# Performance work log

Measured on AMD Instinct MI355X. Metric: run time of the kernel, lower is better.

Reference implementation:

```python
import jax, jax.numpy as jnp
import numpy as np

# Model dims
B, S, D = 2, 1024, 1024          # batch, seq, d_model
NH, HD = 16, 64                  # n_heads, head_dim
E, K, H = 8, 2, 4096             # num_experts, experts_per_token, expert hidden
EPS = 1e-6
ROPE_BASE = 10000.0


def rmsnorm(x, w):
    # RMSNorm: x * rsqrt(mean(x^2) + eps) * weight (no mean-centering, no bias)
    return x * jax.lax.rsqrt(jnp.mean(x * x, axis=-1, keepdims=True) + EPS) * w


def apply_rope(q, k):
    # q,k: [B, NH, S, HD]; position_ids = arange(S) broadcast over batch
    hd = q.shape[-1]
    s = q.shape[2]
    inv_freq = 1.0 / (ROPE_BASE ** (jnp.arange(0, hd, 2, dtype=jnp.float32) / hd))
    freqs = jnp.arange(s, dtype=jnp.float32)[:, None] * inv_freq          # [S, HD/2]
    emb = jnp.concatenate([freqs, freqs], axis=-1)                        # [S, HD]
    cos = jnp.cos(emb)[None, None]                                        # [1,1,S,HD]
    sin = jnp.sin(emb)[None, None]

    def rotate_half(x):
        x1, x2 = jnp.split(x, 2, axis=-1)
        return jnp.concatenate([-x2, x1], axis=-1)

    return q * cos + rotate_half(q) * sin, k * cos + rotate_half(k) * sin


def setup_inputs() -> dict:
    key = jax.random.key(0)
    ks = jax.random.split(key, 9)
    sc = 0.02
    return {
        "x": jax.random.normal(ks[0], (B, S, D), jnp.float32),
        "attn_norm_w": jnp.ones((D,), jnp.float32),
        "wq": jax.random.normal(ks[1], (D, D), jnp.float32) * sc,
        "wk": jax.random.normal(ks[2], (D, D), jnp.float32) * sc,
        "wv": jax.random.normal(ks[3], (D, D), jnp.float32) * sc,
        "wo": jax.random.normal(ks[4], (D, D), jnp.float32) * sc,
        "moe_norm_w": jnp.ones((D,), jnp.float32),
        "gate_w": jax.random.normal(ks[5], (E, D), jnp.float32) * sc,
        "w1": jax.random.normal(ks[6], (E, H, D), jnp.float32) * sc,
        "b1": jnp.zeros((E, H), jnp.float32),
        "w2": jax.random.normal(ks[7], (E, D, H), jnp.float32) * sc,
        "b2": jnp.zeros((E, D), jnp.float32),
    }


def reference(x, attn_norm_w, wq, wk, wv, wo, moe_norm_w, gate_w, w1, b1, w2, b2):
    b, s, d = x.shape
    # --- pre-norm causal self-attention with RoPE (eval mode: no dropout) ---
    t = rmsnorm(x, attn_norm_w)
    q = (t @ wq.T).reshape(b, s, NH, HD).transpose(0, 2, 1, 3)
    k = (t @ wk.T).reshape(b, s, NH, HD).transpose(0, 2, 1, 3)
    v = (t @ wv.T).reshape(b, s, NH, HD).transpose(0, 2, 1, 3)
    q, k = apply_rope(q, k)
    scores = jnp.einsum("bhqd,bhkd->bhqk", q, k) / np.float32(np.sqrt(HD))
    causal = jnp.tril(jnp.ones((s, s), bool))
    scores = jnp.where(causal, scores, jnp.float32(-1e30))
    attn = jax.nn.softmax(scores, axis=-1)
    ao = jnp.einsum("bhqk,bhkd->bhqd", attn, v).transpose(0, 2, 1, 3).reshape(b, s, d)
    h = x + ao @ wo.T

    # --- sparse top-k MoE FFN (internal RMSNorm + residual) ---
    tn = rmsnorm(h, moe_norm_w).reshape(-1, d)                  # [T, D]
    logits = tn @ gate_w.T                                      # [T, E]
    gate_scores, idx = jax.lax.top_k(logits, K)                 # [T, K]
    rw = jax.nn.softmax(gate_scores, axis=-1)                   # [T, K]
    # compute all experts densely, then gather selected (same math as
    # gathering per-token expert weight matrices, far less memory traffic)
    hid = jax.nn.gelu(jnp.einsum("td,ehd->teh", tn, w1) + b1, approximate=False)
    eo = jnp.einsum("teh,edh->ted", hid, w2) + b2               # [T, E, D]
    sel = jnp.take_along_axis(eo, idx[:, :, None], axis=1)      # [T, K, D]
    moe_out = jnp.einsum("tkd,tk->td", sel, rw).reshape(b, s, d)
    return h + moe_out
```

## Files before the change

kernel.cpp:

```cpp
#include <hip/hip_runtime.h>
#include <hip/hip_bf16.h>
#include <hip/hip_fp16.h>


#define T_TOK 2048
#define DMODEL 1024
#define SEQ 1024
#define NEXP 8
#define HEXP 4096

typedef __attribute__((ext_vector_type(4))) float f32x4;
typedef __attribute__((ext_vector_type(4))) int i32x4;
typedef __attribute__((ext_vector_type(8))) short short8;
typedef __attribute__((ext_vector_type(8))) _Float16 half8;
typedef __attribute__((ext_vector_type(4))) _Float16 half4;

#define WAIT_VM3 asm volatile("s_waitcnt vmcnt(3)" ::: "memory")
#define WAIT_VM4 asm volatile("s_waitcnt vmcnt(4)" ::: "memory")
#define WAIT_VM6 asm volatile("s_waitcnt vmcnt(6)" ::: "memory")
#define WAIT_VM0 asm volatile("s_waitcnt vmcnt(0)" ::: "memory")
#define WAIT_LGKM0 asm volatile("s_waitcnt lgkmcnt(0)" ::: "memory")
#define BARRIER __builtin_amdgcn_s_barrier()
#define SCHEDFENCE __builtin_amdgcn_sched_barrier(0)

__device__ __forceinline__ void gload16(const void* g, void* l)
{
    __builtin_amdgcn_global_load_lds((const __attribute__((address_space(1))) void*)g,
                                     (__attribute__((address_space(3))) void*)l, 16, 0, 0);
}

__device__ __forceinline__ void bsplit(float f, unsigned short& hi, unsigned short& lo)
{
    unsigned int u = __float_as_uint(f);
    unsigned int rh = (u + 0x7FFFu + ((u >> 16) & 1u)) >> 16;
    hi = (unsigned short)rh;
    float fl = f - __uint_as_float(rh << 16);
    unsigned int u2 = __float_as_uint(fl);
    lo = (unsigned short)((u2 + 0x7FFFu + ((u2 >> 16) & 1u)) >> 16);
}

__device__ __forceinline__ float gelu_fast(float v)
{
    float e = __expf(-1.5957691216f * v * (1.0f + 0.044715f * v * v));
    return v * __builtin_amdgcn_rcpf(1.0f + e);
}

__global__ __launch_bounds__(256) void split4_kernel(
    const float* __restrict__ s0, const float* __restrict__ s1,
    const float* __restrict__ s2, const float* __restrict__ s3,
    unsigned short* __restrict__ h0, unsigned short* __restrict__ h1,
    unsigned short* __restrict__ h2, unsigned short* __restrict__ h3,
    unsigned short* __restrict__ l0, unsigned short* __restrict__ l1,
    unsigned short* __restrict__ l2, unsigned short* __restrict__ l3, int n4)
{
    int z = blockIdx.y;
    const float* src = (z == 0) ? s0 : (z == 1) ? s1 : (z == 2) ? s2 : s3;
    unsigned short* hi = (z == 0) ? h0 : (z == 1) ? h1 : (z == 2) ? h2 : h3;
    unsigned short* lo = (z == 0) ? l0 : (z == 1) ? l1 : (z == 2) ? l2 : l3;
    int stride = gridDim.x * blockDim.x;
    for (int i = blockIdx.x * blockDim.x + threadIdx.x; i < n4; i += stride) {
        float4 v = ((const float4*)src)[i];
        ushort4 h, l;
        bsplit(v.x, h.x, l.x); bsplit(v.y, h.y, l.y);
        bsplit(v.z, h.z, l.z); bsplit(v.w, h.w, l.w);
        *(ushort4*)(hi + (size_t)i * 4) = h;
        *(ushort4*)(lo + (size_t)i * 4) = l;
    }
}

__global__ __launch_bounds__(256) void rmsnorm_kernel(const float* __restrict__ x,
                                                      const float* __restrict__ w,
                                                      float* __restrict__ of,
                                                      _Float16* __restrict__ oh,
                                                      unsigned short* __restrict__ ohi,
                                                      unsigned short* __restrict__ olo)
{
    int row = blockIdx.x;
    int t = threadIdx.x;
    float4 v = ((const float4*)(x + (size_t)row * DMODEL))[t];
    float ss = v.x * v.x + v.y * v.y + v.z * v.z + v.w * v.w;
#pragma unroll
    for (int off = 32; off > 0; off >>= 1) ss += __shfl_xor(ss, off);
    __shared__ float red[4];
    if ((t & 63) == 0) red[t >> 6] = ss;
    __syncthreads();
    float tot = red[0] + red[1] + red[2] + red[3];
    float sc = rsqrtf(tot * (1.0f / DMODEL) + 1e-6f);
    float4 w4 = ((const float4*)w)[t];
    float4 o;
    o.x = v.x * sc * w4.x; o.y = v.y * sc * w4.y; o.z = v.z * sc * w4.z; o.w = v.w * sc * w4.w;
    if (of) ((float4*)(of + (size_t)row * DMODEL))[t] = o;
    if (oh) {
        half4 h = { (_Float16)o.x, (_Float16)o.y, (_Float16)o.z, (_Float16)o.w };
        *(half4*)(oh + (size_t)row * DMODEL + t * 4) = h;
    }
    if (ohi) {
        ushort4 h, l;
        bsplit(o.x, h.x, l.x); bsplit(o.y, h.y, l.y);
        bsplit(o.z, h.z, l.z); bsplit(o.w, h.w, l.w);
        *(ushort4*)(ohi + (size_t)row * DMODEL + t * 4) = h;
        *(ushort4*)(olo + (size_t)row * DMODEL + t * 4) = l;
    }
}

__global__ __launch_bounds__(256) void gemm_split_kernel(
    const unsigned short* __restrict__ aH, const unsigned short* __restrict__ aL,
    const unsigned short* __restrict__ b0H, const unsigned short* __restrict__ b0L,
    const unsigned short* __restrict__ b1H, const unsigned short* __restrict__ b1L,
    const unsigned short* __restrict__ b2H, const unsigned short* __restrict__ b2L,
    float* __restrict__ C0, float* __restrict__ C1, float* __restrict__ C2,
    const float* __restrict__ resid, int K)
{
    const unsigned short* bH = (blockIdx.z == 0) ? b0H : (blockIdx.z == 1 ? b1H : b2H);
    const unsigned short* bL = (blockIdx.z == 0) ? b0L : (blockIdx.z == 1 ? b1L : b2L);
    float* C = (blockIdx.z == 0) ? C0 : (blockIdx.z == 1 ? C1 : C2);
    int m0 = blockIdx.y * 128, n0 = blockIdx.x * 64;
    __shared__ unsigned short AsH[2][128 * 32];
    __shared__ unsigned short AsL[2][128 * 32];
    __shared__ unsigned short BsH[2][64 * 32];
    __shared__ unsigned short BsL[2][64 * 32];
    int t = threadIdx.x, w = t >> 6, l = t & 63;
    int sa = l >> 2, sc = (l & 3) * 8;
    const unsigned short* gAH0 = aH + (size_t)(m0 + w * 32 + sa) * K + sc;
    const unsigned short* gAH1 = aH + (size_t)(m0 + w * 32 + 16 + sa) * K + sc;
    const unsigned short* gAL0 = aL + (size_t)(m0 + w * 32 + sa) * K + sc;
    const unsigned short* gAL1 = aL + (size_t)(m0 + w * 32 + 16 + sa) * K + sc;
    const unsigned short* gBH0 = bH + (size_t)(n0 + w * 16 + sa) * K + sc;
    const unsigned short* gBL0 = bL + (size_t)(n0 + w * 16 + sa) * K + sc;
    const int aoff0 = (w * 32) * 32;
    const int aoff1 = (w * 32 + 16) * 32;
    const int boff0 = (w * 16) * 32;
    int wr = w >> 1, wc = w & 1;
    f32x4 zero = { 0.0f, 0.0f, 0.0f, 0.0f };
    f32x4 acc[4][2];
#pragma unroll
    for (int i = 0; i < 4; i++)
#pragma unroll
        for (int j = 0; j < 2; j++) acc[i][j] = zero;

#define GS_STAGE(B, K0) do { \
    gload16(gAH0 + (K0), &AsH[B][aoff0]); gload16(gAH1 + (K0), &AsH[B][aoff1]); \
    gload16(gAL0 + (K0), &AsL[B][aoff0]); gload16(gAL1 + (K0), &AsL[B][aoff1]); \
    gload16(gBH0 + (K0), &BsH[B][boff0]); gload16(gBL0 + (K0), &BsL[B][boff0]); \
} while (0)

#define GS_COMPUTE(B) do { \
    short8 ah[4], al[4], bh8[2], bl8[2]; \
    _Pragma("unroll") \
    for (int mi = 0; mi < 4; mi++) { \
        int base = (wr * 64 + mi * 16 + (l & 15)) * 32 + (l >> 4) * 8; \
        ah[mi] = *(const short8*)&AsH[B][base]; \
        al[mi] = *(const short8*)&AsL[B][base]; } \
    _Pragma("unroll") \
    for (int ni = 0; ni < 2; ni++) { \
        int base = (wc * 32 + ni * 16 + (l & 15)) * 32 + (l >> 4) * 8; \
        bh8[ni] = *(const short8*)&BsH[B][base]; \
        bl8[ni] = *(const short8*)&BsL[B][base]; } \
    _Pragma("unroll") \
    for (int mi = 0; mi < 4; mi++) \
        _Pragma("unroll") \
        for (int ni = 0; ni < 2; ni++) { \
            acc[mi][ni] = __builtin_amdgcn_mfma_f32_16x16x32_bf16(ah[mi], bh8[ni], acc[mi][ni], 0, 0, 0); \
            acc[mi][ni] = __builtin_amdgcn_mfma_f32_16x16x32_bf16(ah[mi], bl8[ni], acc[mi][ni], 0, 0, 0); \
            acc[mi][ni] = __builtin_amdgcn_mfma_f32_16x16x32_bf16(al[mi], bh8[ni], acc[mi][ni], 0, 0, 0); } \
} while (0)

    const int nt = K >> 5;
    GS_STAGE(0, 0);
    for (int kt = 0; kt < nt; kt += 2) {
        GS_STAGE(1, (kt + 1) << 5);
        WAIT_VM6;
        BARRIER; SCHEDFENCE;
        GS_COMPUTE(0);
        BARRIER;
        if (kt + 2 < nt) {
            GS_STAGE(0, (kt + 2) << 5);
            WAIT_VM6;
        } else {
            WAIT_VM0;
        }
        BARRIER; SCHEDFENCE;
        GS_COMPUTE(1);
        BARRIER;
    }
#undef GS_STAGE
#undef GS_COMPUTE

#pragma unroll
    for (int mi = 0; mi < 4; mi++) {
#pragma unroll
        for (int r = 0; r < 4; r++) {
            int row = m0 + wr * 64 + mi * 16 + (l >> 4) * 4 + r;
#pragma unroll
            for (int ni = 0; ni < 2; ni++) {
                int col = n0 + wc * 32 + ni * 16 + (l & 15);
                float v = acc[mi][ni][r];
                if (resid) v += resid[(size_t)row * DMODEL + col];
                C[(size_t)row * DMODEL + col] = v;
            }
        }
    }
}

__global__ __launch_bounds__(256) void rope_split_kernel(
    const float* __restrict__ qf, const float* __restrict__ kf,
    unsigned short* __restrict__ qHi, unsigned short* __restrict__ qLo,
    unsigned short* __restrict__ kHi, unsigned short* __restrict__ kLo)
{
    int i = blockIdx.x * 256 + threadIdx.x;
    int tok = i >> 9;
    int r = i & 511;
    int hh = r >> 5, ii = r & 31;
    int s = tok & (SEQ - 1);
    int b = tok >> 10;
    float invf = powf(10000.0f, -(float)(2 * ii) * (1.0f / 64.0f));
    float ang = (float)s * invf;
    float c = cosf(ang), sn = sinf(ang);
    size_t base = (size_t)tok * DMODEL + hh * 64 + ii;
    float q1 = qf[base], q2 = qf[base + 32];
    float k1 = kf[base], k2 = kf[base + 32];
    float rq1 = (q1 * c - q2 * sn) * 0.125f;
    float rq2 = (q2 * c + q1 * sn) * 0.125f;
    float rk1 = k1 * c - k2 * sn;
    float rk2 = k2 * c + k1 * sn;
    int bh = b * 16 + hh;
    size_t qb = ((size_t)bh * SEQ + s) * 64 + ii;
    unsigned short h, lo;
    bsplit(rq1, h, lo); qHi[qb] = h; qLo[qb] = lo;
    bsplit(rq2, h, lo); qHi[qb + 32] = h; qLo[qb + 32] = lo;
    size_t kb = (size_t)bh * (SEQ * 64) + (size_t)(s >> 6) * 4096 + (size_t)(s & 63) * 64;
    int d1 = ii, d2 = ii + 32;
    int p1 = (((d1 >> 3) ^ (s & 7)) << 3) | (d1 & 7);
    int p2 = (((d2 >> 3) ^ (s & 7)) << 3) | (d2 & 7);
    bsplit(rk1, h, lo); kHi[kb + p1] = h; kLo[kb + p1] = lo;
    bsplit(rk2, h, lo); kHi[kb + p2] = h; kLo[kb + p2] = lo;
}

__global__ __launch_bounds__(256) void vtrans_kernel(const float* __restrict__ vf,
                                                     unsigned short* __restrict__ vtHi,
                                                     unsigned short* __restrict__ vtLo)
{
    int sb = blockIdx.x, bh = blockIdx.y;
    int b = bh >> 4, h = bh & 15;
    __shared__ unsigned short tH[64][72];
    __shared__ unsigned short tL[64][72];
    int t = threadIdx.x;
#pragma unroll
    for (int i = 0; i < 4; i++) {
        int idx = i * 256 + t, row = idx >> 4, c4 = idx & 15;
        float4 v = *(const float4*)(vf + (size_t)(b * SEQ + sb * 64 + row) * DMODEL + h * 64 + c4 * 4);
        unsigned short hh, ll;
        bsplit(v.x, hh, ll); tH[c4 * 4 + 0][row] = hh; tL[c4 * 4 + 0][row] = ll;
        bsplit(v.y, hh, ll); tH[c4 * 4 + 1][row] = hh; tL[c4 * 4 + 1][row] = ll;
        bsplit(v.z, hh, ll); tH[c4 * 4 + 2][row] = hh; tL[c4 * 4 + 2][row] = ll;
        bsplit(v.w, hh, ll); tH[c4 * 4 + 3][row] = hh; tL[c4 * 4 + 3][row] = ll;
    }
    __syncthreads();
#pragma unroll
    for (int i = 0; i < 4; i++) {
        int idx = i * 256 + t, d = idx >> 4, sc4 = idx & 15;
        ushort4 oh = { tH[d][sc4 * 4 + 0], tH[d][sc4 * 4 + 1], tH[d][sc4 * 4 + 2], tH[d][sc4 * 4 + 3] };
        ushort4 ol = { tL[d][sc4 * 4 + 0], tL[d][sc4 * 4 + 1], tL[d][sc4 * 4 + 2], tL[d][sc4 * 4 + 3] };
        size_t off = (size_t)bh * (64 * SEQ) + (size_t)sb * 4096 + (size_t)d * 64
                   + (((sc4 >> 1) ^ (d & 7)) << 3) + ((sc4 & 1) << 2);
        *(ushort4*)(vtHi + off) = oh;
        *(ushort4*)(vtLo + off) = ol;
    }
}

__global__ __launch_bounds__(512) void attn_mfma_kernel(
    const unsigned short* __restrict__ qHi, const unsigned short* __restrict__ qLo,
    const unsigned short* __restrict__ kHi, const unsigned short* __restrict__ kLo,
    const unsigned short* __restrict__ vtHi, const unsigned short* __restrict__ vtLo,
    float* __restrict__ Opart, float* __restrict__ mscr, float* __restrict__ lscr)
{
    int qt = 7 - blockIdx.x;
    int bh = blockIdx.y, ks = blockIdx.z;
    int t = threadIdx.x, w = t >> 6, l = t & 63;
    int lq = l & 15, g = l >> 4, lx = lq & 7;
    __shared__ unsigned short KsH[2][4096];
    __shared__ unsigned short KsL[2][4096];
    __shared__ unsigned short VsH[2][4096];
    __shared__ unsigned short VsL[2][4096];
    __shared__ unsigned short PsH[8][1024];
    __shared__ unsigned short PsL[8][1024];
    const size_t hb = (size_t)bh * (SEQ * 64);
    const unsigned short* kHp = kHi + hb;
    const unsigned short* kLp = kLo + hb;
    const unsigned short* vHp = vtHi + hb;
    const unsigned short* vLp = vtLo + hb;
    int qrow = qt * 128 + w * 16 + lq;
    short8 qh[2], qlo8[2];
#pragma unroll
    for (int c = 0; c < 2; c++) {
        size_t off = hb + (size_t)qrow * 64 + c * 32 + g * 8;
        qh[c]   = *(const short8*)(qHi + off);
        qlo8[c] = *(const short8*)(qLo + off);
    }
    f32x4 zero = { 0.0f, 0.0f, 0.0f, 0.0f };
    f32x4 acc_o[4];
#pragma unroll
    for (int i = 0; i < 4; i++) acc_o[i] = zero;
    float mrun = -3.0e38f, lrun = 0.0f;
    int ktl = ks ? (qt + 1) : 0;
    int kth = ks ? (2 * qt + 2) : (qt + 1);

#define AT_STAGE(B, KT) do { \
    size_t so = (size_t)(KT) * 4096 + (w * 64 + l) * 8; \
    gload16(kHp + so, &KsH[B][w * 512]); \
    gload16(kLp + so, &KsL[B][w * 512]); \
    gload16(vHp + so, &VsH[B][w * 512]); \
    gload16(vLp + so, &VsL[B][w * 512]); \
} while (0)

#define AT_COMPUTE(B, KT) do { \
    f32x4 sacc[4]; \
    _Pragma("unroll") \
    for (int i = 0; i < 4; i++) sacc[i] = zero; \
    _Pragma("unroll") \
    for (int nf = 0; nf < 4; nf++) { \
        _Pragma("unroll") \
        for (int c = 0; c < 2; c++) { \
            int ka = (nf * 16 + lq) * 64 + (((c * 4 + g) ^ lx) << 3); \
            short8 kh = *(const short8*)&KsH[B][ka]; \
            short8 kl = *(const short8*)&KsL[B][ka]; \
            sacc[nf] = __builtin_amdgcn_mfma_f32_16x16x32_bf16(kh, qh[c], sacc[nf], 0, 0, 0); \
            sacc[nf] = __builtin_amdgcn_mfma_f32_16x16x32_bf16(kh, qlo8[c], sacc[nf], 0, 0, 0); \
            sacc[nf] = __builtin_amdgcn_mfma_f32_16x16x32_bf16(kl, qh[c], sacc[nf], 0, 0, 0); \
        } \
    } \
    _Pragma("unroll") \
    for (int nf = 0; nf < 4; nf++) \
        _Pragma("unroll") \
        for (int r = 0; r < 4; r++) \
            if ((KT) * 64 + nf * 16 + g * 4 + r > qrow) sacc[nf][r] = -1.0e30f; \
    float mt = sacc[0][0]; \
    _Pragma("unroll") \
    for (int nf = 0; nf < 4; nf++) \
        _Pragma("unroll") \
        for (int r = 0; r < 4; r++) mt = fmaxf(mt, sacc[nf][r]); \
    mt = fmaxf(mt, __shfl_xor(mt, 16)); \
    mt = fmaxf(mt, __shfl_xor(mt, 32)); \
    float mnew = fmaxf(mrun, mt); \
    float p[4][4]; \
    float ps = 0.0f; \
    _Pragma("unroll") \
    for (int nf = 0; nf < 4; nf++) \
        _Pragma("unroll") \
        for (int r = 0; r < 4; r++) { \
            float e = __expf(sacc[nf][r] - mnew); \
            p[nf][r] = e; \
            ps += e; \
        } \
    ps += __shfl_xor(ps, 16); \
    ps += __shfl_xor(ps, 32); \
    float scale = __expf(mrun - mnew); \
    lrun = lrun * scale + ps; \
    mrun = mnew; \
    _Pragma("unroll") \
    for (int nf = 0; nf < 4; nf++) { \
        ushort4 ph, pl; \
        bsplit(p[nf][0], ph.x, pl.x); bsplit(p[nf][1], ph.y, pl.y); \
        bsplit(p[nf][2], ph.z, pl.z); bsplit(p[nf][3], ph.w, pl.w); \
        int pa = lq * 64 + (((nf * 2 + (g >> 1)) ^ lx) << 3) + ((g & 1) << 2); \
        *(ushort4*)&PsH[w][pa] = ph; \
        *(ushort4*)&PsL[w][pa] = pl; \
    } \
    float scq[4]; \
    _Pragma("unroll") \
    for (int r = 0; r < 4; r++) scq[r] = __shfl(scale, g * 4 + r); \
    _Pragma("unroll") \
    for (int df = 0; df < 4; df++) \
        _Pragma("unroll") \
        for (int r = 0; r < 4; r++) acc_o[df][r] *= scq[r]; \
    _Pragma("unroll") \
    for (int c = 0; c < 2; c++) { \
        int pa = lq * 64 + (((c * 4 + g) ^ lx) << 3); \
        short8 ph8 = *(const short8*)&PsH[w][pa]; \
        short8 pl8 = *(const short8*)&PsL[w][pa]; \
        _Pragma("unroll") \
        for (int df = 0; df < 4; df++) { \
            int va = (df * 16 + lq) * 64 + (((c * 4 + g) ^ lx) << 3); \
            short8 vh = *(const short8*)&VsH[B][va]; \
            short8 vl = *(const short8*)&VsL[B][va]; \
            acc_o[df] = __builtin_amdgcn_mfma_f32_16x16x32_bf16(ph8, vh, acc_o[df], 0, 0, 0); \
            acc_o[df] = __builtin_amdgcn_mfma_f32_16x16x32_bf16(ph8, vl, acc_o[df], 0, 0, 0); \
            acc_o[df] = __builtin_amdgcn_mfma_f32_16x16x32_bf16(pl8, vh, acc_o[df], 0, 0, 0); \
        } \
    } \
} while (0)

    int kt = ktl;
    AT_STAGE(0, kt);
    for (; kt + 1 < kth; kt += 2) {
        AT_STAGE(1, kt + 1);
        WAIT_VM4;
        BARRIER; SCHEDFENCE;
        AT_COMPUTE(0, kt);
        BARRIER;
        if (kt + 2 < kth) {
            AT_STAGE(0, kt + 2);
            WAIT_VM4;
        } else {
            WAIT_VM0;
        }
        BARRIER; SCHEDFENCE;
        AT_COMPUTE(1, kt + 1);
        BARRIER;
    }
    if (kt < kth) {
        WAIT_VM0;
        BARRIER; SCHEDFENCE;
        AT_COMPUTE(0, kt);
    }
#undef AT_STAGE
#undef AT_COMPUTE

    if (g == 0) {
        size_t mi = (size_t)(ks * 32 + bh) * SEQ + (size_t)(qt * 128 + w * 16 + lq);
        mscr[mi] = mrun;
        lscr[mi] = lrun;
    }
#pragma unroll
    for (int df = 0; df < 4; df++)
#pragma unroll
        for (int r = 0; r < 4; r++) {
            size_t row = (size_t)(ks * 32 + bh) * SEQ + (size_t)(qt * 128 + w * 16 + g * 4 + r);
            Opart[row * 64 + df * 16 + lq] = acc_o[df][r];
        }
}

__global__ __launch_bounds__(256) void attn_combine_kernel(
    const float* __restrict__ Opart, const float* __restrict__ mscr,
    const float* __restrict__ lscr,
    unsigned short* __restrict__ aoHi, unsigned short* __restrict__ aoLo)
{
    int i = blockIdx.x * 256 + threadIdx.x;
    int d4 = i & 15;
    int qr = (i >> 4) & (SEQ - 1);
    int bh = i >> 14;
    int b = bh >> 4, h = bh & 15;
    size_t r0 = (size_t)bh * SEQ + qr;
    size_t r1 = (size_t)(32 + bh) * SEQ + qr;
    float m0 = mscr[r0], m1 = mscr[r1];
    float l0 = lscr[r0], l1 = lscr[r1];
    float m = fmaxf(m0, m1);
    float w0 = __expf(m0 - m), w1 = __expf(m1 - m);
    float dn = 1.0f / (w0 * l0 + w1 * l1);
    float4 o0 = *(const float4*)(Opart + r0 * 64 + d4 * 4);
    float4 o1 = *(const float4*)(Opart + r1 * 64 + d4 * 4);
    float4 o;
    o.x = (w0 * o0.x + w1 * o1.x) * dn;
    o.y = (w0 * o0.y + w1 * o1.y) * dn;
    o.z = (w0 * o0.z + w1 * o1.z) * dn;
    o.w = (w0 * o0.w + w1 * o1.w) * dn;
    ushort4 hs, ls;
    bsplit(o.x, hs.x, ls.x); bsplit(o.y, hs.y, ls.y);
    bsplit(o.z, hs.z, ls.z); bsplit(o.w, hs.w, ls.w);
    size_t base = (size_t)b * SEQ * DMODEL + (size_t)qr * DMODEL + h * 64 + d4 * 4;
    *(ushort4*)(aoHi + base) = hs;
    *(ushort4*)(aoLo + base) = ls;
}

__global__ __launch_bounds__(256) void gate_kernel(const float* __restrict__ tn2f,
                                                   const float* __restrict__ gw,
                                                   float* __restrict__ logits)
{
    int tok = blockIdx.x;
    int t = threadIdx.x, e = t >> 5, l32 = t & 31;
    const float* xr = tn2f + (size_t)tok * DMODEL;
    const float* gr = gw + (size_t)e * DMODEL;
    float s = 0.0f;
    for (int j = l32; j < DMODEL; j += 32) s += xr[j] * gr[j];
#pragma unroll
    for (int off = 16; off > 0; off >>= 1) s += __shfl_down(s, off, 32);
    if (l32 == 0) logits[tok * NEXP + e] = s;
}

__global__ void zero_kernel(int* p, int n)
{
    int i = blockIdx.x * blockDim.x + threadIdx.x;
    if (i < n) p[i] = 0;
}

__global__ void top2_kernel(const float* __restrict__ logits, float* __restrict__ rw,
                            int* __restrict__ cnt, int* __restrict__ entry)
{
    int t = blockIdx.x * blockDim.x + threadIdx.x;
    if (t >= T_TOK) return;
    float l[8];
#pragma unroll
    for (int e = 0; e < 8; e++) l[e] = logits[t * 8 + e];
    int e0 = 0;
#pragma unroll
    for (int e = 1; e < 8; e++) if (l[e] > l[e0]) e0 = e;
    int e1 = (e0 == 0) ? 1 : 0;
#pragma unroll
    for (int e = 0; e < 8; e++) if (e != e0 && l[e] > l[e1]) e1 = e;
    float ex = expf(l[e1] - l[e0]);
    float denom = 1.0f + ex;
    rw[t * 2 + 0] = 1.0f / denom;
    rw[t * 2 + 1] = ex / denom;
    int pos = atomicAdd(&cnt[e0], 1);
    entry[e0 * 2048 + pos] = t * 2;
    pos = atomicAdd(&cnt[e1], 1);
    entry[e1 * 2048 + pos] = t * 2 + 1;
}

__global__ void offs_kernel(const int* __restrict__ cnt, int* __restrict__ offs)
{
    if (threadIdx.x == 0) {
        int s = 0;
        for (int e = 0; e < 8; e++) { offs[e] = s; s += cnt[e]; }
    }
}

__global__ __launch_bounds__(512) void moe_gemm1_kernel(
    const _Float16* __restrict__ tn2h, const float* __restrict__ w1f,
    const float* __restrict__ b1, const int* __restrict__ cnt, const int* __restrict__ offs,
    const int* __restrict__ entry, _Float16* __restrict__ hid)
{
    int bid = blockIdx.x;
    int e = bid & 7;
    int n_i = (bid >> 3) & 31;
    int m_i = bid >> 8;
    int ne = cnt[e];
    int m0 = m_i * 256;
    if (m0 >= ne) return;
    int n0 = n_i * 128;
    __shared__ _Float16 As[2][256 * 32];
    __shared__ _Float16 Bs[2][128 * 32];
    int t = threadIdx.x, w = t >> 6, l = t & 63;
    int sa = l >> 2;
    int swz = (l >> 3) & 3;
    int scA = ((l & 3) ^ swz) * 8;
    int scB = (l & 3) * 8;
    int rcol = (((l >> 4) ^ ((l >> 1) & 3)) * 8);
    int g0 = entry[e * 2048 + min(m0 + w * 32 + sa, ne - 1)] >> 1;
    int g1 = entry[e * 2048 + min(m0 + w * 32 + 16 + sa, ne - 1)] >> 1;
    const _Float16* gA0 = tn2h + (size_t)g0 * DMODEL + scA;
    const _Float16* gA1 = tn2h + (size_t)g1 * DMODEL + scA;
    const float* w1e = w1f + (size_t)e * HEXP * DMODEL;
    const float* gB0f = w1e + (size_t)(n0 + w * 16 + sa) * DMODEL + scB;
    const int aoff0 = (w * 32) * 32, aoff1 = (w * 32 + 16) * 32;
    const int boff0 = (w * 16 + sa) * 32 + ((l & 3) ^ swz) * 8;
    int wr = w >> 1, wc = w & 1;
    f32x4 zero = { 0.0f, 0.0f, 0.0f, 0.0f };
    f32x4 acc[4][4];
#pragma unroll
    for (int i = 0; i < 4; i++)
#pragma unroll
        for (int j = 0; j < 4; j++) acc[i][j] = zero;
    f32x4 br0, br1;

#define M1_LOADB(K0) do { \
    br0 = *(const f32x4*)(gB0f + (K0)); \
    br1 = *(const f32x4*)(gB0f + (K0) + 4); \
} while (0)

#define M1_STAGE(B, K0) do { \
    half8 hb0 = { (_Float16)br0[0], (_Float16)br0[1], (_Float16)br0[2], (_Float16)br0[3], \
                  (_Float16)br1[0], (_Float16)br1[1], (_Float16)br1[2], (_Float16)br1[3] }; \
    *(half8*)&Bs[B][boff0] = hb0; \
    gload16(gA0 + (K0), &As[B][aoff0]); gload16(gA1 + (K0), &As[B][aoff1]); \
    WAIT_LGKM0; \
} while (0)

#define M1_COMPUTE(B) do { \
    half8 af[4], bfr[4]; \
    _Pragma("unroll") \
    for (int mi = 0; mi < 4; mi++) \
        af[mi] = *(const half8*)&As[B][(wr * 64 + mi * 16 + (l & 15)) * 32 + rcol]; \
    _Pragma("unroll") \
    for (int ni = 0; ni < 4; ni++) \
        bfr[ni] = *(const half8*)&Bs[B][(wc * 64 + ni * 16 + (l & 15)) * 32 + rcol]; \
    _Pragma("unroll") \
    for (int mi = 0; mi < 4; mi++) \
        _Pragma("unroll") \
        for (int ni = 0; ni < 4; ni++) \
            acc[mi][ni] = __builtin_amdgcn_mfma_f32_16x16x32_f16(af[mi], bfr[ni], acc[mi][ni], 0, 0, 0); \
} while (0)

    const int nt = DMODEL >> 5;
    M1_LOADB(0);
    M1_STAGE(0, 0);
    M1_LOADB(32);
    for (int kt = 0; kt < nt; kt += 2) {
        M1_STAGE(1, (kt + 1) << 5);
        if (kt + 2 < nt) M1_LOADB((kt + 2) << 5);
        WAIT_VM4;
        BARRIER; SCHEDFENCE;
        M1_COMPUTE(0);
        BARRIER;
        if (kt + 2 < nt) {
            M1_STAGE(0, (kt + 2) << 5);
            if (kt + 3 < nt) M1_LOADB((kt + 3) << 5);
            WAIT_VM4;
        } else {
            WAIT_VM0;
        }
        BARRIER; SCHEDFENCE;
        M1_COMPUTE(1);
        BARRIER;
    }
#undef M1_LOADB
#undef M1_STAGE
#undef M1_COMPUTE

    int off_e = offs[e];
#pragma unroll
    for (int mi = 0; mi < 4; mi++) {
#pragma unroll
        for (int r = 0; r < 4; r++) {
            int row = m0 + wr * 64 + mi * 16 + (l >> 4) * 4 + r;
            if (row < ne) {
                size_t orow = (size_t)(off_e + row) * HEXP;
#pragma unroll
                for (int ni = 0; ni < 4; ni++) {
                    int cg = n0 + wc * 64 + ni * 16 + (l & 15);
                    float v = acc[mi][ni][r] + b1[e * HEXP + cg];
                    hid[orow + cg] = (_Float16)gelu_fast(v);
                }
            }
        }
    }
}

__global__ __launch_bounds__(512) void moe_gemm2_kernel(
    const _Float16* __restrict__ hid, const float* __restrict__ w2f,
    const float* __restrict__ b2, const int* __restrict__ cnt, const int* __restrict__ offs,
    const int* __restrict__ entry,
    float* __restrict__ eoA, float* __restrict__ eoB,
    float* __restrict__ eoC, float* __restrict__ eoD)
{
    int bid = blockIdx.x;
    int e = bid & 7;
    int rest = bid >> 3;
    int n_i = rest & 7;
    int rest2 = rest >> 3;
    int ks = rest2 & 3;
    int m_i = rest2 >> 2;
    int ne = cnt[e];
    int m0 = m_i * 256;
    if (m0 >= ne) return;
    int n0 = n_i * 128;
    int kbase = ks * (HEXP / 4);
    float* eoP = (ks == 0) ? eoA : (ks == 1) ? eoB : (ks == 2) ? eoC : eoD;
    __shared__ _Float16 As[2][256 * 32];
    __shared__ _Float16 Bs[2][128 * 32];
    int t = threadIdx.x, w = t >> 6, l = t & 63;
    int off_e = offs[e];
    int sa = l >> 2;
    int swz = (l >> 3) & 3;
    int scA = ((l & 3) ^ swz) * 8;
    int scB = (l & 3) * 8;
    int rcol = (((l >> 4) ^ ((l >> 1) & 3)) * 8);
    int r0 = off_e + min(m0 + w * 32 + sa, ne - 1);
    int r1 = off_e + min(m0 + w * 32 + 16 + sa, ne - 1);
    const _Float16* gA0 = hid + (size_t)r0 * HEXP + kbase + scA;
    const _Float16* gA1 = hid + (size_t)r1 * HEXP + kbase + scA;
    const float* w2e = w2f + (size_t)e * DMODEL * HEXP;
    const float* gB0f = w2e + (size_t)(n0 + w * 16 + sa) * HEXP + kbase + scB;
    const int aoff0 = (w * 32) * 32, aoff1 = (w * 32 + 16) * 32;
    const int boff0 = (w * 16 + sa) * 32 + ((l & 3) ^ swz) * 8;
    int wr = w >> 1, wc = w & 1;
    f32x4 zero = { 0.0f, 0.0f, 0.0f, 0.0f };
    f32x4 acc[4][4];
#pragma unroll
    for (int i = 0; i < 4; i++)
#pragma unroll
        for (int j = 0; j < 4; j++) acc[i][j] = zero;
    f32x4 br0, br1;

#define M2_LOADB(K0) do { \
    br0 = *(const f32x4*)(gB0f + (K0)); \
    br1 = *(const f32x4*)(gB0f + (K0) + 4); \
} while (0)

#define M2_STAGE(B, K0) do { \
    half8 hb0 = { (_Float16)br0[0], (_Float16)br0[1], (_Float16)br0[2], (_Float16)br0[3], \
                  (_Float16)br1[0], (_Float16)br1[1], (_Float16)br1[2], (_Float16)br1[3] }; \
    *(half8*)&Bs[B][boff0] = hb0; \
    gload16(gA0 + (K0), &As[B][aoff0]); gload16(gA1 + (K0), &As[B][aoff1]); \
    WAIT_LGKM0; \
} while (0)

#define M2_COMPUTE(B) do { \
    half8 af[4], bfr[4]; \
    _Pragma("unroll") \
    for (int mi = 0; mi < 4; mi++) \
        af[mi] = *(const half8*)&As[B][(wr * 64 + mi * 16 + (l & 15)) * 32 + rcol]; \
    _Pragma("unroll") \
    for (int ni = 0; ni < 4; ni++) \
        bfr[ni] = *(const half8*)&Bs[B][(wc * 64 + ni * 16 + (l & 15)) * 32 + rcol]; \
    _Pragma("unroll") \
    for (int mi = 0; mi < 4; mi++) \
        _Pragma("unroll") \
        for (int ni = 0; ni < 4; ni++) \
            acc[mi][ni] = __builtin_amdgcn_mfma_f32_16x16x32_f16(af[mi], bfr[ni], acc[mi][ni], 0, 0, 0); \
} while (0)

    const int nt = (HEXP / 4) >> 5;
    M2_LOADB(0);
    M2_STAGE(0, 0);
    M2_LOADB(32);
    for (int kt = 0; kt < nt; kt += 2) {
        M2_STAGE(1, (kt + 1) << 5);
        if (kt + 2 < nt) M2_LOADB((kt + 2) << 5);
        WAIT_VM4;
        BARRIER; SCHEDFENCE;
        M2_COMPUTE(0);
        BARRIER;
        if (kt + 2 < nt) {
            M2_STAGE(0, (kt + 2) << 5);
            if (kt + 3 < nt) M2_LOADB((kt + 3) << 5);
            WAIT_VM4;
        } else {
            WAIT_VM0;
        }
        BARRIER; SCHEDFENCE;
        M2_COMPUTE(1);
        BARRIER;
    }
#undef M2_LOADB
#undef M2_STAGE
#undef M2_COMPUTE

#pragma unroll
    for (int mi = 0; mi < 4; mi++) {
#pragma unroll
        for (int r = 0; r < 4; r++) {
            int row = m0 + wr * 64 + mi * 16 + (l >> 4) * 4 + r;
            if (row < ne) {
                int t2k = entry[e * 2048 + row];
#pragma unroll
                for (int ni = 0; ni < 4; ni++) {
                    int cg = n0 + wc * 64 + ni * 16 + (l & 15);
                    float v = acc[mi][ni][r];
                    if (ks == 0) v += b2[e * DMODEL + cg];
                    eoP[(size_t)t2k * DMODEL + cg] = v;
                }
            }
        }
    }
}

__global__ __launch_bounds__(256) void combine_kernel(const float* __restrict__ hf,
                                                      const float* __restrict__ eoA,
                                                      const float* __restrict__ eoB,
                                                      const float* __restrict__ eoC,
                                                      const float* __restrict__ eoD,
                                                      const float* __restrict__ rw,
                                                      float* __restrict__ out)
{
    int i = blockIdx.x * 256 + threadIdx.x;
    int tok = i >> 8;
    int d4 = i & 255;
    float4 hv = ((const float4*)hf)[i];
    float p0 = rw[tok * 2], p1 = rw[tok * 2 + 1];
    size_t i0 = (size_t)(tok * 2) * 256 + d4;
    size_t i1 = (size_t)(tok * 2 + 1) * 256 + d4;
    float4 a0 = ((const float4*)eoA)[i0];
    float4 b0 = ((const float4*)eoB)[i0];
    float4 c0 = ((const float4*)eoC)[i0];
    float4 d0 = ((const float4*)eoD)[i0];
    float4 a1 = ((const float4*)eoA)[i1];
    float4 b1 = ((const float4*)eoB)[i1];
    float4 c1 = ((const float4*)eoC)[i1];
    float4 d1 = ((const float4*)eoD)[i1];
    float4 o;
    o.x = hv.x + p0 * (a0.x + b0.x + c0.x + d0.x) + p1 * (a1.x + b1.x + c1.x + d1.x);
    o.y = hv.y + p0 * (a0.y + b0.y + c0.y + d0.y) + p1 * (a1.y + b1.y + c1.y + d1.y);
    o.z = hv.z + p0 * (a0.z + b0.z + c0.z + d0.z) + p1 * (a1.z + b1.z + c1.z + d1.z);
    o.w = hv.w + p0 * (a0.w + b0.w + c0.w + d0.w) + p1 * (a1.w + b1.w + c1.w + d1.w);
    ((float4*)out)[i] = o;
}

extern "C" void kernel_launch(void* const* d_in, const int* in_sizes, int n_in,
                              void* d_out, int out_size, void* d_ws, size_t ws_size,
                              hipStream_t stream)
{
    const float* x   = (const float*)d_in[0];
    const float* anw = (const float*)d_in[1];
    const float* wq  = (const float*)d_in[2];
    const float* wk  = (const float*)d_in[3];
    const float* wv  = (const float*)d_in[4];
    const float* wo  = (const float*)d_in[5];
    const float* mnw = (const float*)d_in[6];
    const float* gw  = (const float*)d_in[7];
    const float* w1  = (const float*)d_in[8];
    const float* b1  = (const float*)d_in[9];
    const float* w2  = (const float*)d_in[10];
    const float* b2  = (const float*)d_in[11];
    float* out = (float*)d_out;

    char* p = (char*)d_ws;
    auto alloc = [&](size_t bytes) { char* q = p; p += (bytes + 255) & ~(size_t)255; return q; };
    const size_t TD = (size_t)T_TOK * DMODEL;
    unsigned short* tnHi = (unsigned short*)alloc(TD * 2);
    unsigned short* tnLo = (unsigned short*)alloc(TD * 2);
    float*    qf   = (float*)alloc(TD * 4);
    float*    kf   = (float*)alloc(TD * 4);
    float*    vf   = (float*)alloc(TD * 4);
    unsigned short* qHi = (unsigned short*)alloc(TD * 2);
    unsigned short* qLo = (unsigned short*)alloc(TD * 2);
    unsigned short* kHi = (unsigned short*)alloc(TD * 2);
    unsigned short* kLo = (unsigned short*)alloc(TD * 2);
    float*    hf   = (float*)alloc(TD * 4);
    unsigned short* wqH = (unsigned short*)alloc((size_t)DMODEL * DMODEL * 2);
    unsigned short* wqL = (unsigned short*)alloc((size_t)DMODEL * DMODEL * 2);
    unsigned short* wkH = (unsigned short*)alloc((size_t)DMODEL * DMODEL * 2);
    unsigned short* wkL = (unsigned short*)alloc((size_t)DMODEL * DMODEL * 2);
    unsigned short* wvH = (unsigned short*)alloc((size_t)DMODEL * DMODEL * 2);
    unsigned short* wvL = (unsigned short*)alloc((size_t)DMODEL * DMODEL * 2);
    unsigned short* woH = (unsigned short*)alloc((size_t)DMODEL * DMODEL * 2);
    unsigned short* woL = (unsigned short*)alloc((size_t)DMODEL * DMODEL * 2);
    char*     moescr = alloc((size_t)64 * 1024 * 1024);
    _Float16* hid  = (_Float16*)alloc((size_t)4096 * HEXP * 2);
    float*    logits = (float*)alloc((size_t)T_TOK * NEXP * 4);
    float*    rw   = (float*)alloc((size_t)T_TOK * 2 * 4);
    int*      cnt  = (int*)alloc(256);
    int*      offs = (int*)alloc(256);
    int*      entry = (int*)alloc((size_t)NEXP * 2048 * 4);
    float*    mscr = (float*)alloc((size_t)2 * 32 * SEQ * 4);
    float*    lscr = (float*)alloc((size_t)2 * 32 * SEQ * 4);
    (void)ws_size; (void)in_sizes; (void)n_in; (void)out_size;

    unsigned short* vtHi = (unsigned short*)qf;
    unsigned short* vtLo = (unsigned short*)qf + TD;
    float* tn2f = qf;
    unsigned short* aoHi = (unsigned short*)kf;
    unsigned short* aoLo = (unsigned short*)kf + TD;
    _Float16* tn2h = (_Float16*)vf;
    float* eoA = (float*)qHi;
    float* eoB = (float*)wqH;
    float* Opart = (float*)moescr;
    float* eoC = (float*)(moescr + (size_t)32 * 1024 * 1024);
    float* eoD = (float*)(moescr + (size_t)48 * 1024 * 1024);

    split4_kernel<<<dim3(512, 4), 256, 0, stream>>>(wq, wk, wv, wo,
        wqH, wkH, wvH, woH, wqL, wkL, wvL, woL, DMODEL * DMODEL / 4);

    rmsnorm_kernel<<<T_TOK, 256, 0, stream>>>(x, anw, nullptr, (_Float16*)nullptr, tnHi, tnLo);
    gemm_split_kernel<<<dim3(16, 16, 3), 256, 0, stream>>>(
        tnHi, tnLo, wqH, wqL, wkH, wkL, wvH, wvL, qf, kf, vf, nullptr, DMODEL);
    rope_split_kernel<<<4096, 256, 0, stream>>>(qf, kf, qHi, qLo, kHi, kLo);
    vtrans_kernel<<<dim3(16, 32), 256, 0, stream>>>(vf, vtHi, vtLo);
    attn_mfma_kernel<<<dim3(8, 32, 2), 512, 0, stream>>>(qHi, qLo, kHi, kLo, vtHi, vtLo,
                                                         Opart, mscr, lscr);
    attn_combine_kernel<<<2048, 256, 0, stream>>>(Opart, mscr, lscr, aoHi, aoLo);
    gemm_split_kernel<<<dim3(16, 16, 1), 256, 0, stream>>>(
        aoHi, aoLo, woH, woL, woH, woL, woH, woL, hf, hf, hf, x, DMODEL);

    rmsnorm_kernel<<<T_TOK, 256, 0, stream>>>(hf, mnw, tn2f, tn2h, nullptr, nullptr);
    gate_kernel<<<T_TOK, 256, 0, stream>>>(tn2f, gw, logits);
    zero_kernel<<<1, 64, 0, stream>>>(cnt, 8);
    top2_kernel<<<8, 256, 0, stream>>>(logits, rw, cnt, entry);
    offs_kernel<<<1, 1, 0, stream>>>(cnt, offs);
    moe_gemm1_kernel<<<2048, 512, 0, stream>>>(tn2h, w1, b1, cnt, offs, entry, hid);
    moe_gemm2_kernel<<<2048, 512, 0, stream>>>(hid, w2, b2, cnt, offs, entry,
                                               eoA, eoB, eoC, eoD);
    combine_kernel<<<2048, 256, 0, stream>>>(hf, eoA, eoB, eoC, eoD, rw, out);
}
```

Measured before the change: 400.4 us.

## Pre-convert w2 to fp16 inside gemm1 and load it directly in gemm2

The first 256 blocks of the gemm1 launch now convert all of w2 from fp32 to fp16 into a new workspace buffer. gemm2 then fetches B tiles straight into LDS with the same async 16-byte loads it uses for A, instead of loading fp32 into registers, converting, and writing LDS. This takes register staging and its LDS-wait out of gemm2's inner loop and halves its weight bytes. In exchange it adds a full 128MB read plus 64MB write of w2 on every call, overlapped with the gemm1 blocks.

```diff
diff --git a/kernel.cpp b/kernel.cpp
--- a/kernel.cpp
+++ b/kernel.cpp
@@ -518,12 +518,26 @@
 __global__ __launch_bounds__(512) void moe_gemm1_kernel(
     const _Float16* __restrict__ tn2h, const float* __restrict__ w1f,
     const float* __restrict__ b1, const int* __restrict__ cnt, const int* __restrict__ offs,
-    const int* __restrict__ entry, _Float16* __restrict__ hid)
+    const int* __restrict__ entry, _Float16* __restrict__ hid,
+    const float* __restrict__ w2f, _Float16* __restrict__ w2h)
 {
     int bid = blockIdx.x;
-    int e = bid & 7;
-    int n_i = (bid >> 3) & 31;
-    int m_i = bid >> 8;
+    if (bid < 256) {
+        const int n8 = NEXP * HEXP * DMODEL / 8;
+        const int stride = 256 * 512;
+        for (int i = bid * 512 + threadIdx.x; i < n8; i += stride) {
+            float4 a = ((const float4*)w2f)[2 * i];
+            float4 b = ((const float4*)w2f)[2 * i + 1];
+            half8 h = { (_Float16)a.x, (_Float16)a.y, (_Float16)a.z, (_Float16)a.w,
+                        (_Float16)b.x, (_Float16)b.y, (_Float16)b.z, (_Float16)b.w };
+            *(half8*)(w2h + (size_t)i * 8) = h;
+        }
+        return;
+    }
+    int gb = bid - 256;
+    int e = gb & 7;
+    int n_i = (gb >> 3) & 31;
+    int m_i = gb >> 8;
     int ne = cnt[e];
     int m0 = m_i * 256;
     if (m0 >= ne) return;
@@ -627,7 +641,7 @@
 }
 
 __global__ __launch_bounds__(512) void moe_gemm2_kernel(
-    const _Float16* __restrict__ hid, const float* __restrict__ w2f,
+    const _Float16* __restrict__ hid, const _Float16* __restrict__ w2h,
     const float* __restrict__ b2, const int* __restrict__ cnt, const int* __restrict__ offs,
     const int* __restrict__ entry,
     float* __restrict__ eoA, float* __restrict__ eoB,
@@ -653,16 +667,15 @@
     int sa = l >> 2;
     int swz = (l >> 3) & 3;
     int scA = ((l & 3) ^ swz) * 8;
-    int scB = (l & 3) * 8;
-    int rcol = (((l >> 4) ^ ((l >> 1) & 3)) * 8);
+    int rcol = ((l >> 4) ^ ((l >> 1) & 3)) * 8;
     int r0 = off_e + min(m0 + w * 32 + sa, ne - 1);
     int r1 = off_e + min(m0 + w * 32 + 16 + sa, ne - 1);
     const _Float16* gA0 = hid + (size_t)r0 * HEXP + kbase + scA;
     const _Float16* gA1 = hid + (size_t)r1 * HEXP + kbase + scA;
-    const float* w2e = w2f + (size_t)e * DMODEL * HEXP;
-    const float* gB0f = w2e + (size_t)(n0 + w * 16 + sa) * HEXP + kbase + scB;
+    const _Float16* w2e = w2h + (size_t)e * DMODEL * HEXP;
+    const _Float16* gB0 = w2e + (size_t)(n0 + w * 16 + sa) * HEXP + kbase + scA;
     const int aoff0 = (w * 32) * 32, aoff1 = (w * 32 + 16) * 32;
-    const int boff0 = (w * 16 + sa) * 32 + ((l & 3) ^ swz) * 8;
+    const int boff0 = (w * 16) * 32;
     int wr = w >> 1, wc = w & 1;
     f32x4 zero = { 0.0f, 0.0f, 0.0f, 0.0f };
     f32x4 acc[4][4];
@@ -670,19 +683,10 @@
     for (int i = 0; i < 4; i++)
 #pragma unroll
         for (int j = 0; j < 4; j++) acc[i][j] = zero;
-    f32x4 br0, br1;
-
-#define M2_LOADB(K0) do { \
-    br0 = *(const f32x4*)(gB0f + (K0)); \
-    br1 = *(const f32x4*)(gB0f + (K0) + 4); \
-} while (0)
 
 #define M2_STAGE(B, K0) do { \
-    half8 hb0 = { (_Float16)br0[0], (_Float16)br0[1], (_Float16)br0[2], (_Float16)br0[3], \
-                  (_Float16)br1[0], (_Float16)br1[1], (_Float16)br1[2], (_Float16)br1[3] }; \
-    *(half8*)&Bs[B][boff0] = hb0; \
     gload16(gA0 + (K0), &As[B][aoff0]); gload16(gA1 + (K0), &As[B][aoff1]); \
-    WAIT_LGKM0; \
+    gload16(gB0 + (K0), &Bs[B][boff0]); \
 } while (0)
 
 #define M2_COMPUTE(B) do { \
@@ -701,20 +705,16 @@
 } while (0)
 
     const int nt = (HEXP / 4) >> 5;
-    M2_LOADB(0);
     M2_STAGE(0, 0);
-    M2_LOADB(32);
     for (int kt = 0; kt < nt; kt += 2) {
         M2_STAGE(1, (kt + 1) << 5);
-        if (kt + 2 < nt) M2_LOADB((kt + 2) << 5);
-        WAIT_VM4;
+        WAIT_VM3;
         BARRIER; SCHEDFENCE;
         M2_COMPUTE(0);
         BARRIER;
         if (kt + 2 < nt) {
             M2_STAGE(0, (kt + 2) << 5);
-            if (kt + 3 < nt) M2_LOADB((kt + 3) << 5);
-            WAIT_VM4;
+            WAIT_VM3;
         } else {
             WAIT_VM0;
         }
@@ -722,7 +722,6 @@
         M2_COMPUTE(1);
         BARRIER;
     }
-#undef M2_LOADB
 #undef M2_STAGE
 #undef M2_COMPUTE
 
@@ -816,6 +815,7 @@
     unsigned short* woH = (unsigned short*)alloc((size_t)DMODEL * DMODEL * 2);
     unsigned short* woL = (unsigned short*)alloc((size_t)DMODEL * DMODEL * 2);
     char*     moescr = alloc((size_t)64 * 1024 * 1024);
+    _Float16* w2h  = (_Float16*)alloc((size_t)NEXP * HEXP * DMODEL * 2);
     _Float16* hid  = (_Float16*)alloc((size_t)4096 * HEXP * 2);
     float*    logits = (float*)alloc((size_t)T_TOK * NEXP * 4);
     float*    rw   = (float*)alloc((size_t)T_TOK * 2 * 4);
@@ -857,8 +857,9 @@
     zero_kernel<<<1, 64, 0, stream>>>(cnt, 8);
     top2_kernel<<<8, 256, 0, stream>>>(logits, rw, cnt, entry);
     offs_kernel<<<1, 1, 0, stream>>>(cnt, offs);
-    moe_gemm1_kernel<<<2048, 512, 0, stream>>>(tn2h, w1, b1, cnt, offs, entry, hid);
-    moe_gemm2_kernel<<<2048, 512, 0, stream>>>(hid, w2, b2, cnt, offs, entry,
+    moe_gemm1_kernel<<<2304, 512, 0, stream>>>(tn2h, w1, b1, cnt, offs, entry, hid,
+                                               w2, w2h);
+    moe_gemm2_kernel<<<2048, 512, 0, stream>>>(hid, w2h, b2, cnt, offs, entry,
                                                eoA, eoB, eoC, eoD);
     combine_kernel<<<2048, 256, 0, stream>>>(hf, eoA, eoB, eoC, eoD, rw, out);
 }
```

New measurement: 410.4 us. +2.5%, slower.

## Overlap next-stage LDS staging with MFMA compute in MoE expert GEMMs

Applied to the files above, without the earlier changes.

Restructures the double-buffered main loops of both MoE expert GEMMs so the next tile's B write to LDS and async A global-to-LDS load are issued before computing on the current buffer. One barrier per half-iteration is used instead of two. The fp32 B prefetch now uses two register sets, raising register pressure, and the lgkmcnt wait after staging is dropped. Correctness relies on the vmcnt(2) waits and barrier ordering covering the LDS writes.

```diff
diff --git a/kernel.cpp b/kernel.cpp
--- a/kernel.cpp
+++ b/kernel.cpp
@@ -15,6 +15,7 @@
 typedef __attribute__((ext_vector_type(8))) _Float16 half8;
 typedef __attribute__((ext_vector_type(4))) _Float16 half4;
 
+#define WAIT_VM2 asm volatile("s_waitcnt vmcnt(2)" ::: "memory")
 #define WAIT_VM3 asm volatile("s_waitcnt vmcnt(3)" ::: "memory")
 #define WAIT_VM4 asm volatile("s_waitcnt vmcnt(4)" ::: "memory")
 #define WAIT_VM6 asm volatile("s_waitcnt vmcnt(6)" ::: "memory")
@@ -551,19 +552,16 @@
     for (int i = 0; i < 4; i++)
 #pragma unroll
         for (int j = 0; j < 4; j++) acc[i][j] = zero;
-    f32x4 br0, br1;
-
-#define M1_LOADB(K0) do { \
-    br0 = *(const f32x4*)(gB0f + (K0)); \
-    br1 = *(const f32x4*)(gB0f + (K0) + 4); \
-} while (0)
-
-#define M1_STAGE(B, K0) do { \
-    half8 hb0 = { (_Float16)br0[0], (_Float16)br0[1], (_Float16)br0[2], (_Float16)br0[3], \
-                  (_Float16)br1[0], (_Float16)br1[1], (_Float16)br1[2], (_Float16)br1[3] }; \
-    *(half8*)&Bs[B][boff0] = hb0; \
+    f32x4 brA0, brA1, brB0, brB1;
+
+#define M1_WRITEB(B, R0, R1) do { \
+    half8 hb = { (_Float16)R0[0], (_Float16)R0[1], (_Float16)R0[2], (_Float16)R0[3], \
+                 (_Float16)R1[0], (_Float16)R1[1], (_Float16)R1[2], (_Float16)R1[3] }; \
+    *(half8*)&Bs[B][boff0] = hb; \
+} while (0)
+
+#define M1_GLOADA(B, K0) do { \
     gload16(gA0 + (K0), &As[B][aoff0]); gload16(gA1 + (K0), &As[B][aoff1]); \
-    WAIT_LGKM0; \
 } while (0)
 
 #define M1_COMPUTE(B) do { \
@@ -582,29 +580,40 @@
 } while (0)
 
     const int nt = DMODEL >> 5;
-    M1_LOADB(0);
-    M1_STAGE(0, 0);
-    M1_LOADB(32);
+    brA0 = *(const f32x4*)(gB0f);
+    brA1 = *(const f32x4*)(gB0f + 4);
+    M1_WRITEB(0, brA0, brA1);
+    M1_GLOADA(0, 0);
+    brB0 = *(const f32x4*)(gB0f + 32);
+    brB1 = *(const f32x4*)(gB0f + 36);
+    WAIT_VM2;
+    BARRIER; SCHEDFENCE;
     for (int kt = 0; kt < nt; kt += 2) {
-        M1_STAGE(1, (kt + 1) << 5);
-        if (kt + 2 < nt) M1_LOADB((kt + 2) << 5);
-        WAIT_VM4;
+        M1_WRITEB(1, brB0, brB1);
+        M1_GLOADA(1, (kt + 1) << 5);
+        if (kt + 2 < nt) {
+            brA0 = *(const f32x4*)(gB0f + ((kt + 2) << 5));
+            brA1 = *(const f32x4*)(gB0f + ((kt + 2) << 5) + 4);
+        }
+        M1_COMPUTE(0);
+        if (kt + 2 < nt) { WAIT_VM2; } else { WAIT_VM0; }
         BARRIER; SCHEDFENCE;
-        M1_COMPUTE(0);
-        BARRIER;
         if (kt + 2 < nt) {
-            M1_STAGE(0, (kt + 2) << 5);
-            if (kt + 3 < nt) M1_LOADB((kt + 3) << 5);
-            WAIT_VM4;
+            M1_WRITEB(0, brA0, brA1);
+            M1_GLOADA(0, (kt + 2) << 5);
+            if (kt + 3 < nt) {
+                brB0 = *(const f32x4*)(gB0f + ((kt + 3) << 5));
+                brB1 = *(const f32x4*)(gB0f + ((kt + 3) << 5) + 4);
+            }
+            M1_COMPUTE(1);
+            if (kt + 3 < nt) { WAIT_VM2; } else { WAIT_VM0; }
+            BARRIER; SCHEDFENCE;
         } else {
-            WAIT_VM0;
-        }
-        BARRIER; SCHEDFENCE;
-        M1_COMPUTE(1);
-        BARRIER;
-    }
-#undef M1_LOADB
-#undef M1_STAGE
+            M1_COMPUTE(1);
+        }
+    }
+#undef M1_WRITEB
+#undef M1_GLOADA
 #undef M1_COMPUTE
 
     int off_e = offs[e];
@@ -670,19 +679,16 @@
     for (int i = 0; i < 4; i++)
 #pragma unroll
         for (int j = 0; j < 4; j++) acc[i][j] = zero;
-    f32x4 br0, br1;
-
-#define M2_LOADB(K0) do { \
-    br0 = *(const f32x4*)(gB0f + (K0)); \
-    br1 = *(const f32x4*)(gB0f + (K0) + 4); \
-} while (0)
-
-#define M2_STAGE(B, K0) do { \
-    half8 hb0 = { (_Float16)br0[0], (_Float16)br0[1], (_Float16)br0[2], (_Float16)br0[3], \
-                  (_Float16)br1[0], (_Float16)br1[1], (_Float16)br1[2], (_Float16)br1[3] }; \
-    *(half8*)&Bs[B][boff0] = hb0; \
+    f32x4 brA0, brA1, brB0, brB1;
+
+#define M2_WRITEB(B, R0, R1) do { \
+    half8 hb = { (_Float16)R0[0], (_Float16)R0[1], (_Float16)R0[2], (_Float16)R0[3], \
+                 (_Float16)R1[0], (_Float16)R1[1], (_Float16)R1[2], (_Float16)R1[3] }; \
+    *(half8*)&Bs[B][boff0] = hb; \
+} while (0)
+
+#define M2_GLOADA(B, K0) do { \
     gload16(gA0 + (K0), &As[B][aoff0]); gload16(gA1 + (K0), &As[B][aoff1]); \
-    WAIT_LGKM0; \
 } while (0)
 
 #define M2_COMPUTE(B) do { \
@@ -701,29 +707,40 @@
 } while (0)
 
     const int nt = (HEXP / 4) >> 5;
-    M2_LOADB(0);
-    M2_STAGE(0, 0);
-    M2_LOADB(32);
+    brA0 = *(const f32x4*)(gB0f);
+    brA1 = *(const f32x4*)(gB0f + 4);
+    M2_WRITEB(0, brA0, brA1);
+    M2_GLOADA(0, 0);
+    brB0 = *(const f32x4*)(gB0f + 32);
+    brB1 = *(const f32x4*)(gB0f + 36);
+    WAIT_VM2;
+    BARRIER; SCHEDFENCE;
     for (int kt = 0; kt < nt; kt += 2) {
-        M2_STAGE(1, (kt + 1) << 5);
-        if (kt + 2 < nt) M2_LOADB((kt + 2) << 5);
-        WAIT_VM4;
+        M2_WRITEB(1, brB0, brB1);
+        M2_GLOADA(1, (kt + 1) << 5);
+        if (kt + 2 < nt) {
+            brA0 = *(const f32x4*)(gB0f + ((kt + 2) << 5));
+            brA1 = *(const f32x4*)(gB0f + ((kt + 2) << 5) + 4);
+        }
+        M2_COMPUTE(0);
+        if (kt + 2 < nt) { WAIT_VM2; } else { WAIT_VM0; }
         BARRIER; SCHEDFENCE;
-        M2_COMPUTE(0);
-        BARRIER;
         if (kt + 2 < nt) {
-            M2_STAGE(0, (kt + 2) << 5);
-            if (kt + 3 < nt) M2_LOADB((kt + 3) << 5);
-            WAIT_VM4;
+            M2_WRITEB(0, brA0, brA1);
+            M2_GLOADA(0, (kt + 2) << 5);
+            if (kt + 3 < nt) {
+                brB0 = *(const f32x4*)(gB0f + ((kt + 3) << 5));
+                brB1 = *(const f32x4*)(gB0f + ((kt + 3) << 5) + 4);
+            }
+            M2_COMPUTE(1);
+            if (kt + 3 < nt) { WAIT_VM2; } else { WAIT_VM0; }
+            BARRIER; SCHEDFENCE;
         } else {
-            WAIT_VM0;
-        }
-        BARRIER; SCHEDFENCE;
-        M2_COMPUTE(1);
-        BARRIER;
-    }
-#undef M2_LOADB
-#undef M2_STAGE
+            M2_COMPUTE(1);
+        }
+    }
+#undef M2_WRITEB
+#undef M2_GLOADA
 #undef M2_COMPUTE
 
 #pragma unroll
```

After: 450.6 us. +12.5%, slower.
